# Kernel tuning notes

Hardware: AMD Instinct MI355X
Metric: run time of the kernel (lower is better)

## Reference

```python
import jax, jax.numpy as jnp
import numpy as np
import math

E = 2048; H = 16; NOPE = 128; ROPE = 64; VH = 128; C = 512; QR = 1536
DR = 2; BASE = 10000.0; LR = 4  # hypernet low_rank -> C//4 = 128
B = 2; S = 2048


def _ln(x, g, b):
    m = jnp.mean(x, axis=-1, keepdims=True)
    v = jnp.mean((x - m) ** 2, axis=-1, keepdims=True)
    return (x - m) / jnp.sqrt(v + 1e-5) * g + b


def _rope(x, sin, cos):
    # interleaved rotary: x[..., 0::2], x[..., 1::2]
    x1 = x[..., 0::2]
    x2 = x[..., 1::2]
    out = jnp.stack([x1 * cos - x2 * sin, x1 * sin + x2 * cos], axis=-1)
    return out.reshape(x.shape)


def _sincos(pos, dim):
    inv = BASE ** (-jnp.arange(0, dim, 2, dtype=jnp.float32) / dim)
    ang = pos[:, None] * inv  # [S, dim//2]
    return jnp.sin(ang), jnp.cos(ang)


def _pe(T, d):
    # sinusoidal positional encoding [T, d]
    pos = jnp.arange(T, dtype=jnp.float32)[:, None]
    div = jnp.exp(jnp.arange(0, d, 2, dtype=jnp.float32) * (-math.log(10000.0) / d))
    pe = jnp.zeros((T, d))
    pe = pe.at[:, 0::2].set(jnp.sin(pos * div))
    pe = pe.at[:, 1::2].set(jnp.cos(pos * div))
    return pe


def _forward(query, key, value, wq_a, q_ln_g, q_ln_b, wq_b, wkv_a, kv_ln_g,
             kv_ln_b, wkv_b, wo, fc_c_w, fc_c_b, fc_p_w, fc_p_b, pos_scale):
    B_, S_, _ = query.shape
    # LoRA query path
    ql = _ln(query @ wq_a.T, q_ln_g, q_ln_b)                 # [B,S,QR]
    q = (ql @ wq_b.T).reshape(B_, S_, H, NOPE + ROPE)
    q_nope, q_pe = q[..., :NOPE], q[..., NOPE:]
    # positions: start_pos = key_len - 1 (prefill entering incremental path)
    start = S_ - 1
    pos = jnp.arange(start, start + S_, dtype=jnp.float32)
    sin, cos = _sincos(pos, ROPE)                            # [S, ROPE//2]
    q_pe = _rope(q_pe, sin[None, :, None, :], cos[None, :, None, :])
    # KV latent path
    kvf = key @ wkv_a.T                                      # [B,S,C+ROPE]
    kv, k_pe = kvf[..., :C], kvf[..., C:]
    k_pe = _rope(k_pe, sin[None, :, :], cos[None, :, :])     # [B,S,ROPE]
    kvn = _ln(kv, kv_ln_g, kv_ln_b)                          # [B,S,C]
    # HyperNetwork temporal compression: W [B, t, T]
    T = S_
    t = math.ceil(T / DR)
    Cpe = _pe(t, C)                                          # [t, C]
    C2 = Cpe @ fc_c_w.T + fc_c_b                             # [t, C//LR]
    P2 = kvn @ fc_p_w.T + fc_p_b                             # [B,T,C//LR]
    W = jax.nn.sigmoid(jnp.einsum('tr,bTr->btT', C2, P2))    # [B,t,T]
    # chunk mask: compressed slot r gathers tokens in its down_rate chunk
    zm = (jnp.arange(T)[None, :] // DR == jnp.arange(t)[:, None]).astype(kvn.dtype)
    prev_kv = jnp.einsum('btT,bTc->btc', W * zm[None], kvn)  # [B,t,C]
    idx = list(range(DR - 1, T, DR))
    if T - 1 not in idx:
        idx.append(T - 1)
    prev_kpe = k_pe[:, np.array(idx)]                        # [B,t,ROPE]
    # LoRA-absorbed attention
    wkvb = wkv_b.reshape(H, NOPE + VH, C)
    qn = jnp.einsum('bshd,hdc->bshc', q_nope, wkvb[:, :NOPE])
    content = jnp.einsum('bshc,btc->bsht', qn, prev_kv)
    # decoupled (normalized) rope scores
    qpe_n = q_pe / jnp.maximum(jnp.linalg.norm(q_pe, axis=-1, keepdims=True), 1e-12)
    kpe_n = prev_kpe / jnp.maximum(jnp.linalg.norm(prev_kpe, axis=-1, keepdims=True), 1e-12)
    pscore = jnp.einsum('bshr,btr->bsht', qpe_n, kpe_n)
    scores = (content + pos_scale * pscore) * ((NOPE + ROPE) ** -0.5)
    attn = jax.nn.softmax(scores, axis=-1)                   # [B,S,H,t]
    x = jnp.einsum('bsht,btc->bshc', attn, prev_kv)
    x = jnp.einsum('bshc,hdc->bshd', x, wkvb[:, NOPE:])      # value up-proj
    return x.reshape(B_, S_, H * VH) @ wo.T


def setup_inputs() -> dict:
    key = jax.random.key(0)
    ks = jax.random.split(key, 16)
    s = 0.02
    return {
        'query': jax.random.normal(ks[0], (B, S, E), jnp.float32),
        'key': jax.random.normal(ks[1], (B, S, E), jnp.float32),
        'value': jax.random.normal(ks[2], (B, S, E), jnp.float32),
        'wq_a': jax.random.normal(ks[3], (QR, E), jnp.float32) * s,
        'q_ln_g': jnp.ones((QR,), jnp.float32),
        'q_ln_b': jnp.zeros((QR,), jnp.float32),
        'wq_b': jax.random.normal(ks[4], (H * (NOPE + ROPE), QR), jnp.float32) * s,
        'wkv_a': jax.random.normal(ks[5], (C + ROPE, E), jnp.float32) * s,
        'kv_ln_g': jnp.ones((C,), jnp.float32),
        'kv_ln_b': jnp.zeros((C,), jnp.float32),
        'wkv_b': jax.random.normal(ks[6], (H * (NOPE + VH), C), jnp.float32) * s,
        'wo': jax.random.normal(ks[7], (E, H * VH), jnp.float32) * s,
        'fc_c_w': jax.random.normal(ks[8], (C // LR, C), jnp.float32) * s,
        'fc_c_b': jnp.zeros((C // LR,), jnp.float32),
        'fc_p_w': jax.random.normal(ks[9], (C // LR, C), jnp.float32) * s,
        'fc_p_b': jnp.zeros((C // LR,), jnp.float32),
        'pos_scale': jnp.asarray(1.0, jnp.float32),
    }


def reference(query, key, value, wq_a, q_ln_g, q_ln_b, wq_b, wkv_a, kv_ln_g,
              kv_ln_b, wkv_b, wo, fc_c_w, fc_c_b, fc_p_w, fc_p_b, pos_scale):
    return _forward(query, key, value, wq_a, q_ln_g, q_ln_b, wq_b, wkv_a,
                    kv_ln_g, kv_ln_b, wkv_b, wo, fc_c_w, fc_c_b, fc_p_w,
                    fc_p_b, pos_scale)
```

## Files before the change

kernel.cpp:

```cpp
#include <hip/hip_runtime.h>
#include <math.h>

#define S_ 2048
#define B_ 2
#define H_ 16
#define E_ 2048
#define QR_ 1536
#define NOPE_ 128
#define ROPE_ 64
#define C_ 512
#define VH_ 128
#define T_ 1024
#define LN1E4 9.210340371976184f
#define SCALE_ 0.07216878364870323f

typedef _Float16 half8 __attribute__((ext_vector_type(8)));
typedef _Float16 half4 __attribute__((ext_vector_type(4)));
typedef __fp16 fp16x2 __attribute__((ext_vector_type(2)));
typedef float floatx4 __attribute__((ext_vector_type(4)));
#define MFMA16(a, b, c) __builtin_amdgcn_mfma_f32_16x16x32_f16(a, b, c, 0, 0, 0)

__device__ __forceinline__ void gload16(const _Float16* g, _Float16* l) {
  __builtin_amdgcn_global_load_lds(
      (__attribute__((address_space(1))) const void*)g,
      (__attribute__((address_space(3))) void*)l, 16, 0, 0);
}

__device__ __forceinline__ int xcd_swizzle(int orig, int nwg) {
  int q8 = nwg >> 3, r8 = nwg & 7, xcd = orig & 7, base = orig >> 3;
  return (xcd < r8 ? xcd * (q8 + 1) : r8 * (q8 + 1) + (xcd - r8) * q8) + base;
}

__global__ __launch_bounds__(256) void conv_all(
    const float* __restrict__ q, const float* __restrict__ k,
    const float* __restrict__ wqa, const float* __restrict__ wqb,
    const float* __restrict__ wkva, const float* __restrict__ wo,
    const float* __restrict__ fcc, const float* __restrict__ fcp,
    const float* __restrict__ wkvb,
    _Float16* q16, _Float16* k16, _Float16* wqa16, _Float16* wqb16,
    _Float16* wkva16, _Float16* wo16, _Float16* fcc16, _Float16* fcp16,
    _Float16* W1c, _Float16* W2c)
{
  size_t i = (size_t)blockIdx.x * 256 + threadIdx.x;
  if (i >= 3768320) {
    bool isW1 = i < 3899392;
    size_t j = i - (isW1 ? 3768320 : 3899392);
    int cch = j & 63, hd = (int)(j >> 6);
    int hh = hd >> 7, dd = hd & 127;
    const float* src = wkvb + ((size_t)(hh * 256 + (isW1 ? 0 : 128) + dd)) * 512 + cch * 8;
    float sc = isW1 ? SCALE_ : 1.f;
    float4 a = *(const float4*)src;
    float4 b = *(const float4*)(src + 4);
    half8 h = {(_Float16)(a.x * sc), (_Float16)(a.y * sc), (_Float16)(a.z * sc),
               (_Float16)(a.w * sc), (_Float16)(b.x * sc), (_Float16)(b.y * sc),
               (_Float16)(b.z * sc), (_Float16)(b.w * sc)};
    *(half8*)((isW1 ? W1c : W2c) + j * 8) = h;
    return;
  }
  const float* in; _Float16* out; size_t off;
  if      (i < 1048576) { in = q;    out = q16;    off = i; }
  else if (i < 2097152) { in = k;    out = k16;    off = i - 1048576; }
  else if (i < 2490368) { in = wqa;  out = wqa16;  off = i - 2097152; }
  else if (i < 3080192) { in = wqb;  out = wqb16;  off = i - 2490368; }
  else if (i < 3227648) { in = wkva; out = wkva16; off = i - 3080192; }
  else if (i < 3751936) { in = wo;   out = wo16;   off = i - 3227648; }
  else if (i < 3760128) { in = fcc;  out = fcc16;  off = i - 3751936; }
  else                  { in = fcp;  out = fcp16;  off = i - 3760128; }
  float4 a = ((const float4*)in)[2 * off];
  float4 b = ((const float4*)in)[2 * off + 1];
  half8 h = {(_Float16)a.x, (_Float16)a.y, (_Float16)a.z, (_Float16)a.w,
             (_Float16)b.x, (_Float16)b.y, (_Float16)b.z, (_Float16)b.w};
  *(half8*)(out + 8 * off) = h;
}

template<bool OUT16, bool NB, bool BIAS, bool TRANSC, bool DUAL = false>
__global__ __launch_bounds__(256) void gemm16(
    const _Float16* __restrict__ A, const _Float16* __restrict__ Bm,
    const float* __restrict__ bias, const float* __restrict__ bias2,
    float* __restrict__ Cf, _Float16* __restrict__ Ch,
    int N, int K, int lda, int ldb, int ldc,
    long sAb, long sAh, long sBb, long sBh, long sCb, long sCh)
{
  __shared__ __align__(16) _Float16 Asl[2][128 * 64];
  __shared__ __align__(16) _Float16 Bsl[2][128 * 64];
  int mode = 0;
  if (DUAL) {
    int zz = blockIdx.z;
    mode = zz >> 5;
    int z2 = zz & 31;
    int zb2 = z2 >> 4, zh2 = z2 & 15;
    A += (size_t)zb2 * sAb;
    const _Float16* Bsel = mode ? (const _Float16*)bias2 : Bm;
    Bm = Bsel + (size_t)zh2 * (128 * C_);
    if (mode) Ch = ((_Float16*)Cf) + ((size_t)(zb2 * H_ + zh2) * 128) * T_;
    else      Ch += ((size_t)(zb2 * H_ + zh2) * T_) * 192;
  } else {
    const int z = blockIdx.z, zb = z >> 4, zh = z & 15;
    A  += (size_t)zb * sAb + (size_t)zh * sAh;
    Bm += (size_t)zb * sBb + (size_t)zh * sBh;
    if (OUT16) Ch += (size_t)zb * sCb + (size_t)zh * sCh;
    else       Cf += (size_t)zb * sCb + (size_t)zh * sCh;
  }
  const int gx = gridDim.x;
  const int nwg = gx * gridDim.y;
  const int f = xcd_swizzle(blockIdx.y * gx + blockIdx.x, nwg);
  const int bm = (f / gx) * 128, bn = (f % gx) * 128;
  const int tid = threadIdx.x;
  const int w = tid >> 6, lane = tid & 63, l15 = lane & 15, g = lane >> 4;
  const int wm = (w >> 1) * 64, wn = (w & 1) * 64;
  const int srow = w * 32 + (lane >> 3);
  const int sch  = (lane & 7) ^ (lane >> 3);
  floatx4 acc[4][4];
  #pragma unroll
  for (int i = 0; i < 4; ++i)
    #pragma unroll
    for (int j = 0; j < 4; ++j) acc[i][j] = (floatx4){0.f, 0.f, 0.f, 0.f};

  auto STAGE = [&](int buf, int k0) {
    _Float16* al = &Asl[buf][w * 2048];
    _Float16* bl = &Bsl[buf][w * 2048];
    #pragma unroll
    for (int i = 0; i < 4; ++i)
      gload16(A + (size_t)(bm + srow + i * 8) * lda + k0 + sch * 8, al + i * 512);
    #pragma unroll
    for (int i = 0; i < 4; ++i)
      gload16(Bm + (size_t)(bn + srow + i * 8) * ldb + k0 + sch * 8, bl + i * 512);
  };

  STAGE(0, 0);
  int cur = 0;
  const int nIter = K >> 6;
  for (int it = 0; it < nIter; ++it) {
    const bool pf = (it + 1 < nIter);
    if (pf) STAGE(cur ^ 1, (it + 1) << 6);
    if (pf) asm volatile("s_waitcnt vmcnt(8)" ::: "memory");
    else    asm volatile("s_waitcnt vmcnt(0)" ::: "memory");
    __builtin_amdgcn_sched_barrier(0);
    __builtin_amdgcn_s_barrier();
    __builtin_amdgcn_sched_barrier(0);
    #pragma unroll
    for (int kk = 0; kk < 2; ++kk) {
      half8 af[4], bf[4];
      const int sw = ((kk * 4 + g) ^ (l15 & 7)) * 8;
      #pragma unroll
      for (int i = 0; i < 4; ++i) {
        af[i] = *(const half8*)&Asl[cur][(wm + i * 16 + l15) * 64 + sw];
        bf[i] = *(const half8*)&Bsl[cur][(wn + i * 16 + l15) * 64 + sw];
      }
      #pragma unroll
      for (int i = 0; i < 4; ++i)
        #pragma unroll
        for (int j = 0; j < 4; ++j)
          acc[i][j] = MFMA16(af[i], bf[j], acc[i][j]);
    }
    asm volatile("s_waitcnt lgkmcnt(0)" ::: "memory");
    __builtin_amdgcn_sched_barrier(0);
    __builtin_amdgcn_s_barrier();
    __builtin_amdgcn_sched_barrier(0);
    cur ^= 1;
  }

  if (DUAL) {
    if (mode) {
      #pragma unroll
      for (int i = 0; i < 4; ++i)
        #pragma unroll
        for (int j = 0; j < 4; ++j) {
          int row = bm + wm + i * 16 + g * 4;
          int col = wn + j * 16 + l15;
          half4 v = {(_Float16)acc[i][j][0], (_Float16)acc[i][j][1],
                     (_Float16)acc[i][j][2], (_Float16)acc[i][j][3]};
          *(half4*)(Ch + (size_t)col * T_ + row) = v;
        }
    } else {
      #pragma unroll
      for (int i = 0; i < 4; ++i)
        #pragma unroll
        for (int j = 0; j < 4; ++j)
          #pragma unroll
          for (int r = 0; r < 4; ++r) {
            int row = bm + wm + i * 16 + g * 4 + r;
            int col = wn + j * 16 + l15;
            Ch[(size_t)row * 192 + col] = (_Float16)acc[i][j][r];
          }
    }
  } else if (TRANSC) {
    #pragma unroll
    for (int i = 0; i < 4; ++i)
      #pragma unroll
      for (int j = 0; j < 4; ++j) {
        int row = bm + wm + i * 16 + g * 4;
        int col = bn + wn + j * 16 + l15;
        half4 v = {(_Float16)acc[i][j][0], (_Float16)acc[i][j][1],
                   (_Float16)acc[i][j][2], (_Float16)acc[i][j][3]};
        *(half4*)(Ch + (size_t)col * ldc + row) = v;
      }
  } else {
    #pragma unroll
    for (int i = 0; i < 4; ++i)
      #pragma unroll
      for (int j = 0; j < 4; ++j)
        #pragma unroll
        for (int r = 0; r < 4; ++r) {
          int row = bm + wm + i * 16 + g * 4 + r;
          int col = bn + wn + j * 16 + l15;
          if (!NB || col < N) {
            float v = acc[i][j][r];
            if (BIAS) v += (col < 128) ? bias[col] : bias2[col - 128];
            if (OUT16) Ch[(size_t)row * ldc + col] = (_Float16)v;
            else       Cf[(size_t)row * ldc + col] = v;
          }
        }
  }
}

template<typename TIN, bool OUT16>
__global__ __launch_bounds__(256) void ln_rows(
    const TIN* __restrict__ in, float* __restrict__ outf, _Float16* __restrict__ outh,
    const float* __restrict__ g, const float* __restrict__ bb,
    int L, int ldin, int ldout)
{
  const int row = blockIdx.x;
  const TIN* x = in + (size_t)row * ldin;
  float s = 0.f, s2 = 0.f;
  for (int i = threadIdx.x; i < L; i += 256) {
    float v = (float)x[i]; s += v; s2 += v * v;
  }
  #pragma unroll
  for (int off = 32; off; off >>= 1) {
    s  += __shfl_xor(s, off, 64);
    s2 += __shfl_xor(s2, off, 64);
  }
  __shared__ float rs[4], rs2[4];
  int lane = threadIdx.x & 63, w = threadIdx.x >> 6;
  if (lane == 0) { rs[w] = s; rs2[w] = s2; }
  __syncthreads();
  s  = rs[0] + rs[1] + rs[2] + rs[3];
  s2 = rs2[0] + rs2[1] + rs2[2] + rs2[3];
  float mean = s / L;
  float var = s2 / L - mean * mean;
  float inv = rsqrtf(var + 1e-5f);
  for (int i = threadIdx.x; i < L; i += 256) {
    float v = ((float)x[i] - mean) * inv * g[i] + bb[i];
    if (OUT16) outh[(size_t)row * ldout + i] = (_Float16)v;
    else       outf[(size_t)row * ldout + i] = v;
  }
}

__global__ __launch_bounds__(256) void rope_q16(_Float16* __restrict__ qb,
                                                const float* __restrict__ ps_ptr)
{
  const int row = blockIdx.x;
  const int s = row & (S_ - 1);
  const int lane = threadIdx.x & 63, w = threadIdx.x >> 6;
  float sn = 0.f, cs = 0.f;
  if (lane < 32) {
    float invf = expf(-(float)lane * (LN1E4 / 32.f));
    float ang = (float)(S_ - 1 + s) * invf;
    sincosf(ang, &sn, &cs);
  }
  const float psc = ps_ptr[0] * SCALE_;
  #pragma unroll
  for (int hh = 0; hh < 4; ++hh) {
    const int h = w + hh * 4;
    _Float16* p = qb + (size_t)row * 3072 + h * 192 + NOPE_;
    float o1 = 0.f, o2 = 0.f;
    if (lane < 32) {
      float x1 = (float)p[2 * lane], x2 = (float)p[2 * lane + 1];
      o1 = x1 * cs - x2 * sn;
      o2 = x1 * sn + x2 * cs;
    }
    float ss = o1 * o1 + o2 * o2;
    #pragma unroll
    for (int off = 32; off; off >>= 1) ss += __shfl_xor(ss, off, 64);
    float inv = psc / fmaxf(sqrtf(ss), 1e-12f);
    if (lane < 32) {
      p[2 * lane]     = (_Float16)(o1 * inv);
      p[2 * lane + 1] = (_Float16)(o2 * inv);
    }
  }
}

__global__ __launch_bounds__(64) void rope_k16(
    const _Float16* __restrict__ kvf16, _Float16* __restrict__ keff)
{
  const int t = blockIdx.x, b = blockIdx.y;
  const int srow = 2 * t + 1;
  const _Float16* p = kvf16 + ((size_t)(b * S_ + srow)) * 576 + C_;
  const int j = threadIdx.x;
  float o1 = 0.f, o2 = 0.f;
  if (j < 32) {
    float invf = expf(-(float)j * (LN1E4 / 32.f));
    float ang = (float)(S_ - 1 + srow) * invf;
    float sn, cs; sincosf(ang, &sn, &cs);
    float x1 = (float)p[2 * j], x2 = (float)p[2 * j + 1];
    o1 = x1 * cs - x2 * sn;
    o2 = x1 * sn + x2 * cs;
  }
  float ss = o1 * o1 + o2 * o2;
  #pragma unroll
  for (int off = 32; off; off >>= 1) ss += __shfl_xor(ss, off, 64);
  float nrm = fmaxf(sqrtf(ss), 1e-12f);
  if (j < 32) {
    _Float16 h1 = (_Float16)(o1 / nrm), h2 = (_Float16)(o2 / nrm);
    #pragma unroll
    for (int h = 0; h < H_; ++h) {
      _Float16* o = keff + ((size_t)((b * H_ + h) * T_) + t) * 192 + NOPE_;
      o[2 * j] = h1; o[2 * j + 1] = h2;
    }
  }
}

__global__ __launch_bounds__(256) void pe16(_Float16* __restrict__ Cpe16)
{
  const int t = blockIdx.x;
  const int i = threadIdx.x;
  float dv = expf(-(float)(2 * i) * (LN1E4 / 512.f));
  float ang = (float)t * dv;
  float sn, cs; sincosf(ang, &sn, &cs);
  Cpe16[(size_t)t * C_ + 2 * i]     = (_Float16)sn;
  Cpe16[(size_t)t * C_ + 2 * i + 1] = (_Float16)cs;
}

__global__ __launch_bounds__(64) void gate_kernel(
    const _Float16* __restrict__ Ccat, const _Float16* __restrict__ kvn16,
    _Float16* __restrict__ pkv16)
{
  const int t = blockIdx.x, b = blockIdx.y;
  const int j = threadIdx.x;
  const _Float16* c2 = Ccat + (size_t)t * 256;
  const _Float16* p0 = Ccat + (size_t)(1024 + b * S_ + 2 * t) * 256 + 128;
  const _Float16* p1 = p0 + 256;
  float d0 = (float)c2[j] * (float)p0[j] + (float)c2[j + 64] * (float)p0[j + 64];
  float d1 = (float)c2[j] * (float)p1[j] + (float)c2[j + 64] * (float)p1[j + 64];
  #pragma unroll
  for (int off = 32; off; off >>= 1) {
    d0 += __shfl_xor(d0, off, 64);
    d1 += __shfl_xor(d1, off, 64);
  }
  float w0 = 1.f / (1.f + expf(-d0));
  float w1 = 1.f / (1.f + expf(-d1));
  const _Float16* k0 = kvn16 + ((size_t)(b * S_ + 2 * t)) * C_;
  const _Float16* k1 = k0 + C_;
  _Float16* o = pkv16 + ((size_t)(b * T_ + t)) * C_;
  #pragma unroll
  for (int it = 0; it < 2; ++it) {
    int c = j * 4 + it * 256;
    half4 a = *(const half4*)(k0 + c);
    half4 bb = *(const half4*)(k1 + c);
    half4 r;
    #pragma unroll
    for (int u = 0; u < 4; ++u)
      r[u] = (_Float16)(w0 * (float)a[u] + w1 * (float)bb[u]);
    *(half4*)(o + c) = r;
  }
}

__global__ __launch_bounds__(256, 3) void attn_flash(
    const _Float16* __restrict__ qb16, const _Float16* __restrict__ keff,
    const _Float16* __restrict__ vT, _Float16* __restrict__ x216)
{
  __shared__ __align__(16) _Float16 K_lds[64 * 192];
  __shared__ __align__(16) _Float16 V_lds[128 * 64];
  const int f = xcd_swizzle(blockIdx.x, 1024);
  const int st = f & 31, h = (f >> 5) & 15, b = f >> 9;
  const int tid = threadIdx.x, w = tid >> 6, lane = tid & 63;
  const int l15 = lane & 15, g = lane >> 4, l7 = lane & 7;
  const int rq = b * S_ + st * 64 + w * 16;
  const _Float16* qrow = qb16 + (size_t)(rq + l15) * 3072 + h * 192;
  half8 qB[6];
  #pragma unroll
  for (int kk = 0; kk < 6; ++kk) qB[kk] = *(const half8*)(qrow + kk * 32 + g * 8);
  floatx4 O[8];
  #pragma unroll
  for (int i = 0; i < 8; ++i) O[i] = (floatx4){0.f, 0.f, 0.f, 0.f};
  float m = -3e38f, l = 0.f;
  const _Float16* kb = keff + (size_t)(b * H_ + h) * T_ * 192;
  const _Float16* vb = vT   + (size_t)(b * H_ + h) * 128 * T_;

  int ksrc[6], ksw[6], vsrc[4], vsw[4];
  #pragma unroll
  for (int p = 0; p < 6; ++p) {
    int c = tid + p * 256;
    int r = c / 24, dc = c % 24;
    ksrc[p] = r * 192 + dc * 8;
    ksw[p]  = r * 192 + ((dc ^ (r & 7)) * 8);
  }
  #pragma unroll
  for (int p = 0; p < 4; ++p) {
    int c = tid + p * 256;
    int r = c >> 3, dc = c & 7;
    vsrc[p] = r * T_ + dc * 8;
    vsw[p]  = r * 64 + ((dc ^ (r & 7)) * 8);
  }
  int kswr[6], vswr[2];
  #pragma unroll
  for (int kk = 0; kk < 6; ++kk) kswr[kk] = ((kk * 4 + g) ^ l7) * 8;
  #pragma unroll
  for (int kc = 0; kc < 2; ++kc) vswr[kc] = ((kc * 4 + g) ^ l7) * 8;

  half8 kreg[6], vreg[4];
  #pragma unroll
  for (int p = 0; p < 6; ++p) kreg[p] = *(const half8*)(kb + ksrc[p]);
  #pragma unroll
  for (int p = 0; p < 4; ++p) vreg[p] = *(const half8*)(vb + vsrc[p]);
  #pragma unroll
  for (int p = 0; p < 6; ++p) *(half8*)&K_lds[ksw[p]] = kreg[p];
  #pragma unroll
  for (int p = 0; p < 4; ++p) *(half8*)&V_lds[vsw[p]] = vreg[p];
  __syncthreads();

  const int srcA = l15 + ((g & 1) << 5);
  const int srcB = srcA + 16;
  const bool hi = (g >> 1) != 0;

  for (int kt = 0; kt < 16; ++kt) {
    if (kt < 15) {
      const int t1 = (kt + 1) * 64;
      #pragma unroll
      for (int p = 0; p < 6; ++p)
        kreg[p] = *(const half8*)(kb + (size_t)t1 * 192 + ksrc[p]);
      #pragma unroll
      for (int p = 0; p < 4; ++p)
        vreg[p] = *(const half8*)(vb + t1 + vsrc[p]);
    }
    floatx4 sc[4];
    #pragma unroll
    for (int i = 0; i < 4; ++i) sc[i] = (floatx4){0.f, 0.f, 0.f, 0.f};
    __builtin_amdgcn_s_setprio(1);
    #pragma unroll
    for (int kk = 0; kk < 6; ++kk)
      #pragma unroll
      for (int ct = 0; ct < 4; ++ct)
        sc[ct] = MFMA16(
            *(const half8*)&K_lds[(ct * 16 + l15) * 192 + kswr[kk]],
            qB[kk], sc[ct]);
    __builtin_amdgcn_s_setprio(0);
    float pm = sc[0][0];
    #pragma unroll
    for (int ct = 0; ct < 4; ++ct)
      #pragma unroll
      for (int r = 0; r < 4; ++r) pm = fmaxf(pm, sc[ct][r]);
    pm = fmaxf(pm, __shfl_xor(pm, 16, 64));
    pm = fmaxf(pm, __shfl_xor(pm, 32, 64));
    int ok = pm <= m + 8.f;
    if (!__all(ok)) {
      float mn = fmaxf(m, pm);
      float sf = __expf(m - mn);
      m = mn; l *= sf;
      float sfO[4];
      #pragma unroll
      for (int r = 0; r < 4; ++r) sfO[r] = __shfl(sf, g * 4 + r, 64);
      #pragma unroll
      for (int cc = 0; cc < 8; ++cc) {
        O[cc][0] *= sfO[0]; O[cc][1] *= sfO[1];
        O[cc][2] *= sfO[2]; O[cc][3] *= sfO[3];
      }
    }
    float rs = 0.f;
    #pragma unroll
    for (int ct = 0; ct < 4; ++ct)
      #pragma unroll
      for (int r = 0; r < 4; ++r) {
        float e = __expf(sc[ct][r] - m);
        sc[ct][r] = e; rs += e;
      }
    rs += __shfl_xor(rs, 16, 64);
    rs += __shfl_xor(rs, 32, 64);
    l += rs;
    unsigned pk[4][2];
    #pragma unroll
    for (int ct = 0; ct < 4; ++ct) {
      union { fp16x2 h; unsigned u; } c0, c1;
      c0.h = __builtin_amdgcn_cvt_pkrtz(sc[ct][0], sc[ct][1]);
      c1.h = __builtin_amdgcn_cvt_pkrtz(sc[ct][2], sc[ct][3]);
      pk[ct][0] = c0.u; pk[ct][1] = c1.u;
    }
    __builtin_amdgcn_s_setprio(1);
    #pragma unroll
    for (int kc = 0; kc < 2; ++kc) {
      unsigned a0 = __shfl((int)pk[2 * kc][0], srcA, 64);
      unsigned b0 = __shfl((int)pk[2 * kc + 1][0], srcA, 64);
      unsigned a1 = __shfl((int)pk[2 * kc][1], srcA, 64);
      unsigned b1 = __shfl((int)pk[2 * kc + 1][1], srcA, 64);
      unsigned a2 = __shfl((int)pk[2 * kc][0], srcB, 64);
      unsigned b2 = __shfl((int)pk[2 * kc + 1][0], srcB, 64);
      unsigned a3 = __shfl((int)pk[2 * kc][1], srcB, 64);
      unsigned b3 = __shfl((int)pk[2 * kc + 1][1], srcB, 64);
      union { unsigned u[4]; half8 h; } pa;
      pa.u[0] = hi ? b0 : a0;
      pa.u[1] = hi ? b1 : a1;
      pa.u[2] = hi ? b2 : a2;
      pa.u[3] = hi ? b3 : a3;
      #pragma unroll
      for (int cc = 0; cc < 8; ++cc)
        O[cc] = MFMA16(pa.h,
            *(const half8*)&V_lds[(cc * 16 + l15) * 64 + vswr[kc]], O[cc]);
    }
    __builtin_amdgcn_s_setprio(0);
    if (kt < 15) {
      __syncthreads();
      #pragma unroll
      for (int p = 0; p < 6; ++p) *(half8*)&K_lds[ksw[p]] = kreg[p];
      #pragma unroll
      for (int p = 0; p < 4; ++p) *(half8*)&V_lds[vsw[p]] = vreg[p];
      __syncthreads();
    }
  }
  float il = 1.f / l;
  float ilO[4];
  #pragma unroll
  for (int r = 0; r < 4; ++r) ilO[r] = __shfl(il, g * 4 + r, 64);
  #pragma unroll
  for (int cc = 0; cc < 8; ++cc)
    #pragma unroll
    for (int r = 0; r < 4; ++r)
      x216[(size_t)(rq + g * 4 + r) * 2048 + h * 128 + cc * 16 + l15] =
          (_Float16)(O[cc][r] * ilO[r]);
}

extern "C" void kernel_launch(void* const* d_in, const int* in_sizes, int n_in,
                              void* d_out, int out_size, void* d_ws, size_t ws_size,
                              hipStream_t stream)
{
  (void)in_sizes; (void)n_in; (void)out_size; (void)ws_size;
  const float* query  = (const float*)d_in[0];
  const float* key    = (const float*)d_in[1];
  const float* wq_a   = (const float*)d_in[3];
  const float* q_ln_g = (const float*)d_in[4];
  const float* q_ln_b = (const float*)d_in[5];
  const float* wq_b   = (const float*)d_in[6];
  const float* wkv_a  = (const float*)d_in[7];
  const float* kv_ln_g= (const float*)d_in[8];
  const float* kv_ln_b= (const float*)d_in[9];
  const float* wkvb   = (const float*)d_in[10];
  const float* wo     = (const float*)d_in[11];
  const float* fc_c_w = (const float*)d_in[12];
  const float* fc_c_b = (const float*)d_in[13];
  const float* fc_p_w = (const float*)d_in[14];
  const float* fc_p_b = (const float*)d_in[15];
  const float* ps     = (const float*)d_in[16];
  float* out = (float*)d_out;

  const int M = B_ * S_;
  _Float16* hws   = (_Float16*)d_ws;
  _Float16* q16   = hws;
  _Float16* key16 = q16   + (size_t)8388608;
  _Float16* wqa16 = key16 + (size_t)8388608;
  _Float16* wqb16 = wqa16 + (size_t)3145728;
  _Float16* wkva16= wqb16 + (size_t)4718592;
  _Float16* wo16  = wkva16+ (size_t)1179648;
  _Float16* ql16  = wo16  + (size_t)4194304;
  _Float16* qb16  = ql16  + (size_t)6291456;
  _Float16* kvf16 = qb16  + (size_t)12582912;
  _Float16* kvn16 = kvf16 + (size_t)2359296;
  _Float16* fcc16 = kvn16 + (size_t)2097152;
  _Float16* fcp16 = fcc16 + (size_t)65536;
  _Float16* W1c   = fcp16 + (size_t)65536;
  _Float16* W2c   = W1c   + (size_t)1048576;
  _Float16* x216  = q16;
  _Float16* keff  = key16;
  _Float16* Cpe16 = kvn16 - (size_t)524288;
  _Float16* Ccat  = wqb16;
  _Float16* pkv16 = wkva16;
  _Float16* vT    = ql16;

  conv_all<<<15744, 256, 0, stream>>>(query, key, wq_a, wq_b, wkv_a, wo, fc_c_w, fc_p_w,
                                      wkvb, q16, key16, wqa16, wqb16, wkva16, wo16,
                                      fcc16, fcp16, W1c, W2c);
  gemm16<true,false,false,false><<<dim3(QR_/128, M/128), 256, 0, stream>>>(
      q16, wqa16, nullptr, nullptr, nullptr, ql16, QR_, E_, E_, E_, QR_, 0,0,0,0,0,0);
  ln_rows<_Float16,true><<<M, 256, 0, stream>>>(ql16, nullptr, ql16, q_ln_g, q_ln_b,
                                                QR_, QR_, QR_);
  gemm16<true,false,false,false><<<dim3(3072/128, M/128), 256, 0, stream>>>(
      ql16, wqb16, nullptr, nullptr, nullptr, qb16, 3072, QR_, QR_, QR_, 3072, 0,0,0,0,0,0);
  rope_q16<<<M, 256, 0, stream>>>(qb16, ps);
  gemm16<true,true,false,false><<<dim3(5, M/128), 256, 0, stream>>>(
      key16, wkva16, nullptr, nullptr, nullptr, kvf16, 576, E_, E_, E_, 576, 0,0,0,0,0,0);
  ln_rows<_Float16,true><<<M, 256, 0, stream>>>(kvf16, nullptr, kvn16, kv_ln_g, kv_ln_b,
                                                C_, 576, C_);
  rope_k16<<<dim3(T_, B_), 64, 0, stream>>>(kvf16, keff);
  pe16<<<T_, 256, 0, stream>>>(Cpe16);
  gemm16<true,false,true,false><<<dim3(2, 5120/128), 256, 0, stream>>>(
      Cpe16, fcc16, fc_c_b, fc_p_b, nullptr, Ccat, 256, C_, C_, C_, 256, 0,0,0,0,0,0);
  gate_kernel<<<dim3(T_, B_), 64, 0, stream>>>(Ccat, kvn16, pkv16);
  gemm16<true,false,false,false,true><<<dim3(1, T_/128, 64), 256, 0, stream>>>(
      pkv16, W1c, nullptr, (const float*)W2c, (float*)vT, keff,
      128, C_, C_, C_, 192, (long)T_*C_, 0L, 0L, 0L, 0L, 0L);
  attn_flash<<<dim3(1024), 256, 0, stream>>>(qb16, keff, vT, x216);
  gemm16<false,false,false,false><<<dim3(E_/128, M/128), 256, 0, stream>>>(
      x216, wo16, nullptr, nullptr, out, nullptr, E_, E_, E_, E_, E_, 0,0,0,0,0,0);
}
```

Baseline: 345.2 us.

## Batch independent GEMMs and elementwise kernels into fewer multi-task launches

Independent GEMMs (q-down with kv-down, and q-up with hypernet C-projection) are merged into one launch each through a task-dispatching gemm_pair kernel. The two layernorms, k-rope and PE generation are merged into one kernel, and q-rope is merged with the gating kernel. Workspace buffers are reassigned so the merged stages do not alias. The aim is to cut launch count and fill the GPU better with small GEMMs running next to large ones. The cost is more branching and a generic GEMM without the templated specialisations.

```diff
diff --git a/kernel.cpp b/kernel.cpp
--- a/kernel.cpp
+++ b/kernel.cpp
@@ -214,58 +214,142 @@
   }
 }
 
-template<typename TIN, bool OUT16>
-__global__ __launch_bounds__(256) void ln_rows(
-    const TIN* __restrict__ in, float* __restrict__ outf, _Float16* __restrict__ outh,
-    const float* __restrict__ g, const float* __restrict__ bb,
-    int L, int ldin, int ldout)
+struct GTask {
+  const _Float16* A; const _Float16* B; _Float16* C;
+  const float* b1; const float* b2;
+  int gx, N, K, lda, ldb, ldc;
+};
+
+__global__ __launch_bounds__(256) void gemm_pair(GTask ta, GTask tb, int n0, int n1)
 {
-  const int row = blockIdx.x;
-  const TIN* x = in + (size_t)row * ldin;
-  float s = 0.f, s2 = 0.f;
-  for (int i = threadIdx.x; i < L; i += 256) {
-    float v = (float)x[i]; s += v; s2 += v * v;
-  }
-  #pragma unroll
-  for (int off = 32; off; off >>= 1) {
-    s  += __shfl_xor(s, off, 64);
-    s2 += __shfl_xor(s2, off, 64);
-  }
+  __shared__ __align__(16) _Float16 Asl[2][128 * 64];
+  __shared__ __align__(16) _Float16 Bsl[2][128 * 64];
+  const bool second = blockIdx.x >= (unsigned)n0;
+  GTask t = second ? tb : ta;
+  const int fid = second ? blockIdx.x - n0 : blockIdx.x;
+  const int nwg = second ? n1 : n0;
+  const int f = xcd_swizzle(fid, nwg);
+  const int bm = (f / t.gx) * 128, bn = (f % t.gx) * 128;
+  const int tid = threadIdx.x;
+  const int w = tid >> 6, lane = tid & 63, l15 = lane & 15, g = lane >> 4;
+  const int wm = (w >> 1) * 64, wn = (w & 1) * 64;
+  const int srow = w * 32 + (lane >> 3);
+  const int sch  = (lane & 7) ^ (lane >> 3);
+  floatx4 acc[4][4];
+  #pragma unroll
+  for (int i = 0; i < 4; ++i)
+    #pragma unroll
+    for (int j = 0; j < 4; ++j) acc[i][j] = (floatx4){0.f, 0.f, 0.f, 0.f};
+
+  auto STAGE = [&](int buf, int k0) {
+    _Float16* al = &Asl[buf][w * 2048];
+    _Float16* bl = &Bsl[buf][w * 2048];
+    #pragma unroll
+    for (int i = 0; i < 4; ++i)
+      gload16(t.A + (size_t)(bm + srow + i * 8) * t.lda + k0 + sch * 8, al + i * 512);
+    #pragma unroll
+    for (int i = 0; i < 4; ++i)
+      gload16(t.B + (size_t)(bn + srow + i * 8) * t.ldb + k0 + sch * 8, bl + i * 512);
+  };
+
+  STAGE(0, 0);
+  int cur = 0;
+  const int nIter = t.K >> 6;
+  for (int it = 0; it < nIter; ++it) {
+    const bool pf = (it + 1 < nIter);
+    if (pf) STAGE(cur ^ 1, (it + 1) << 6);
+    if (pf) asm volatile("s_waitcnt vmcnt(8)" ::: "memory");
+    else    asm volatile("s_waitcnt vmcnt(0)" ::: "memory");
+    __builtin_amdgcn_sched_barrier(0);
+    __builtin_amdgcn_s_barrier();
+    __builtin_amdgcn_sched_barrier(0);
+    #pragma unroll
+    for (int kk = 0; kk < 2; ++kk) {
+      half8 af[4], bf[4];
+      const int sw = ((kk * 4 + g) ^ (l15 & 7)) * 8;
+      #pragma unroll
+      for (int i = 0; i < 4; ++i) {
+        af[i] = *(const half8*)&Asl[cur][(wm + i * 16 + l15) * 64 + sw];
+        bf[i] = *(const half8*)&Bsl[cur][(wn + i * 16 + l15) * 64 + sw];
+      }
+      #pragma unroll
+      for (int i = 0; i < 4; ++i)
+        #pragma unroll
+        for (int j = 0; j < 4; ++j)
+          acc[i][j] = MFMA16(af[i], bf[j], acc[i][j]);
+    }
+    asm volatile("s_waitcnt lgkmcnt(0)" ::: "memory");
+    __builtin_amdgcn_sched_barrier(0);
+    __builtin_amdgcn_s_barrier();
+    __builtin_amdgcn_sched_barrier(0);
+    cur ^= 1;
+  }
+  #pragma unroll
+  for (int i = 0; i < 4; ++i)
+    #pragma unroll
+    for (int j = 0; j < 4; ++j)
+      #pragma unroll
+      for (int r = 0; r < 4; ++r) {
+        int row = bm + wm + i * 16 + g * 4 + r;
+        int col = bn + wn + j * 16 + l15;
+        if (col < t.N) {
+          float v = acc[i][j][r];
+          if (t.b1) v += (col < 128) ? t.b1[col] : t.b2[col - 128];
+          t.C[(size_t)row * t.ldc + col] = (_Float16)v;
+        }
+      }
+}
+
+__global__ __launch_bounds__(256) void fused_ln(
+    _Float16* __restrict__ ql16, const _Float16* __restrict__ kvf16,
+    _Float16* __restrict__ kvnA,
+    const float* __restrict__ qg, const float* __restrict__ qb,
+    const float* __restrict__ kg, const float* __restrict__ kb,
+    _Float16* __restrict__ keff, _Float16* __restrict__ Cpe16)
+{
   __shared__ float rs[4], rs2[4];
-  int lane = threadIdx.x & 63, w = threadIdx.x >> 6;
-  if (lane == 0) { rs[w] = s; rs2[w] = s2; }
-  __syncthreads();
-  s  = rs[0] + rs[1] + rs[2] + rs[3];
-  s2 = rs2[0] + rs2[1] + rs2[2] + rs2[3];
-  float mean = s / L;
-  float var = s2 / L - mean * mean;
-  float inv = rsqrtf(var + 1e-5f);
-  for (int i = threadIdx.x; i < L; i += 256) {
-    float v = ((float)x[i] - mean) * inv * g[i] + bb[i];
-    if (OUT16) outh[(size_t)row * ldout + i] = (_Float16)v;
-    else       outf[(size_t)row * ldout + i] = v;
-  }
-}
-
-__global__ __launch_bounds__(256) void rope_q16(_Float16* __restrict__ qb,
-                                                const float* __restrict__ ps_ptr)
-{
-  const int row = blockIdx.x;
-  const int s = row & (S_ - 1);
-  const int lane = threadIdx.x & 63, w = threadIdx.x >> 6;
-  float sn = 0.f, cs = 0.f;
-  if (lane < 32) {
-    float invf = expf(-(float)lane * (LN1E4 / 32.f));
-    float ang = (float)(S_ - 1 + s) * invf;
-    sincosf(ang, &sn, &cs);
-  }
-  const float psc = ps_ptr[0] * SCALE_;
-  #pragma unroll
-  for (int hh = 0; hh < 4; ++hh) {
-    const int h = w + hh * 4;
-    _Float16* p = qb + (size_t)row * 3072 + h * 192 + NOPE_;
+  int bid = blockIdx.x;
+  const int tid = threadIdx.x;
+  const int lane = tid & 63, w = tid >> 6;
+  if (bid < 8192) {
+    const bool isQ = bid < 4096;
+    const int row = isQ ? bid : bid - 4096;
+    const _Float16* x = isQ ? ql16 + (size_t)row * 1536 : kvf16 + (size_t)row * 576;
+    _Float16* o = isQ ? ql16 + (size_t)row * 1536 : kvnA + (size_t)row * 512;
+    const float* g_ = isQ ? qg : kg;
+    const float* b_ = isQ ? qb : kb;
+    const int L = isQ ? 1536 : 512;
+    float s = 0.f, s2 = 0.f;
+    for (int i = tid; i < L; i += 256) {
+      float v = (float)x[i]; s += v; s2 += v * v;
+    }
+    #pragma unroll
+    for (int off = 32; off; off >>= 1) {
+      s  += __shfl_xor(s, off, 64);
+      s2 += __shfl_xor(s2, off, 64);
+    }
+    if (lane == 0) { rs[w] = s; rs2[w] = s2; }
+    __syncthreads();
+    s  = rs[0] + rs[1] + rs[2] + rs[3];
+    s2 = rs2[0] + rs2[1] + rs2[2] + rs2[3];
+    float mean = s / L;
+    float var = s2 / L - mean * mean;
+    float inv = rsqrtf(var + 1e-5f);
+    for (int i = tid; i < L; i += 256)
+      o[i] = (_Float16)(((float)x[i] - mean) * inv * g_[i] + b_[i]);
+    return;
+  }
+  bid -= 8192;
+  if (bid < 512) {
+    int u = bid * 4 + w;
+    int t = u & (T_ - 1), b = u >> 10;
+    const int srow = 2 * t + 1;
+    const _Float16* p = kvf16 + ((size_t)(b * S_ + srow)) * 576 + C_;
     float o1 = 0.f, o2 = 0.f;
     if (lane < 32) {
+      float invf = expf(-(float)lane * (LN1E4 / 32.f));
+      float ang = (float)(S_ - 1 + srow) * invf;
+      float sn, cs; sincosf(ang, &sn, &cs);
       float x1 = (float)p[2 * lane], x2 = (float)p[2 * lane + 1];
       o1 = x1 * cs - x2 * sn;
       o2 = x1 * sn + x2 * cs;
@@ -273,86 +357,98 @@
     float ss = o1 * o1 + o2 * o2;
     #pragma unroll
     for (int off = 32; off; off >>= 1) ss += __shfl_xor(ss, off, 64);
-    float inv = psc / fmaxf(sqrtf(ss), 1e-12f);
+    float nrm = fmaxf(sqrtf(ss), 1e-12f);
     if (lane < 32) {
-      p[2 * lane]     = (_Float16)(o1 * inv);
-      p[2 * lane + 1] = (_Float16)(o2 * inv);
-    }
-  }
-}
-
-__global__ __launch_bounds__(64) void rope_k16(
-    const _Float16* __restrict__ kvf16, _Float16* __restrict__ keff)
-{
-  const int t = blockIdx.x, b = blockIdx.y;
-  const int srow = 2 * t + 1;
-  const _Float16* p = kvf16 + ((size_t)(b * S_ + srow)) * 576 + C_;
-  const int j = threadIdx.x;
-  float o1 = 0.f, o2 = 0.f;
-  if (j < 32) {
-    float invf = expf(-(float)j * (LN1E4 / 32.f));
-    float ang = (float)(S_ - 1 + srow) * invf;
+      _Float16 h1 = (_Float16)(o1 / nrm), h2 = (_Float16)(o2 / nrm);
+      #pragma unroll
+      for (int h = 0; h < H_; ++h) {
+        _Float16* o = keff + ((size_t)((b * H_ + h) * T_) + t) * 192 + NOPE_;
+        o[2 * lane] = h1; o[2 * lane + 1] = h2;
+      }
+    }
+    return;
+  }
+  bid -= 512;
+  {
+    const int t = bid;
+    float dv = expf(-(float)(2 * tid) * (LN1E4 / 512.f));
+    float ang = (float)t * dv;
     float sn, cs; sincosf(ang, &sn, &cs);
-    float x1 = (float)p[2 * j], x2 = (float)p[2 * j + 1];
-    o1 = x1 * cs - x2 * sn;
-    o2 = x1 * sn + x2 * cs;
-  }
-  float ss = o1 * o1 + o2 * o2;
-  #pragma unroll
-  for (int off = 32; off; off >>= 1) ss += __shfl_xor(ss, off, 64);
-  float nrm = fmaxf(sqrtf(ss), 1e-12f);
-  if (j < 32) {
-    _Float16 h1 = (_Float16)(o1 / nrm), h2 = (_Float16)(o2 / nrm);
-    #pragma unroll
-    for (int h = 0; h < H_; ++h) {
-      _Float16* o = keff + ((size_t)((b * H_ + h) * T_) + t) * 192 + NOPE_;
-      o[2 * j] = h1; o[2 * j + 1] = h2;
-    }
-  }
-}
-
-__global__ __launch_bounds__(256) void pe16(_Float16* __restrict__ Cpe16)
-{
-  const int t = blockIdx.x;
-  const int i = threadIdx.x;
-  float dv = expf(-(float)(2 * i) * (LN1E4 / 512.f));
-  float ang = (float)t * dv;
-  float sn, cs; sincosf(ang, &sn, &cs);
-  Cpe16[(size_t)t * C_ + 2 * i]     = (_Float16)sn;
-  Cpe16[(size_t)t * C_ + 2 * i + 1] = (_Float16)cs;
-}
-
-__global__ __launch_bounds__(64) void gate_kernel(
-    const _Float16* __restrict__ Ccat, const _Float16* __restrict__ kvn16,
+    Cpe16[(size_t)t * C_ + 2 * tid]     = (_Float16)sn;
+    Cpe16[(size_t)t * C_ + 2 * tid + 1] = (_Float16)cs;
+  }
+}
+
+__global__ __launch_bounds__(256) void fused_rq_gate(
+    _Float16* __restrict__ qb16, const float* __restrict__ ps_ptr,
+    const _Float16* __restrict__ Ccat, const _Float16* __restrict__ kvnA,
     _Float16* __restrict__ pkv16)
 {
-  const int t = blockIdx.x, b = blockIdx.y;
-  const int j = threadIdx.x;
-  const _Float16* c2 = Ccat + (size_t)t * 256;
-  const _Float16* p0 = Ccat + (size_t)(1024 + b * S_ + 2 * t) * 256 + 128;
-  const _Float16* p1 = p0 + 256;
-  float d0 = (float)c2[j] * (float)p0[j] + (float)c2[j + 64] * (float)p0[j + 64];
-  float d1 = (float)c2[j] * (float)p1[j] + (float)c2[j + 64] * (float)p1[j + 64];
-  #pragma unroll
-  for (int off = 32; off; off >>= 1) {
-    d0 += __shfl_xor(d0, off, 64);
-    d1 += __shfl_xor(d1, off, 64);
-  }
-  float w0 = 1.f / (1.f + expf(-d0));
-  float w1 = 1.f / (1.f + expf(-d1));
-  const _Float16* k0 = kvn16 + ((size_t)(b * S_ + 2 * t)) * C_;
-  const _Float16* k1 = k0 + C_;
-  _Float16* o = pkv16 + ((size_t)(b * T_ + t)) * C_;
-  #pragma unroll
-  for (int it = 0; it < 2; ++it) {
-    int c = j * 4 + it * 256;
-    half4 a = *(const half4*)(k0 + c);
-    half4 bb = *(const half4*)(k1 + c);
-    half4 r;
-    #pragma unroll
-    for (int u = 0; u < 4; ++u)
-      r[u] = (_Float16)(w0 * (float)a[u] + w1 * (float)bb[u]);
-    *(half4*)(o + c) = r;
+  int bid = blockIdx.x;
+  const int tid = threadIdx.x;
+  const int lane = tid & 63, w = tid >> 6;
+  if (bid < 4096) {
+    const int row = bid;
+    const int s = row & (S_ - 1);
+    float sn = 0.f, cs = 0.f;
+    if (lane < 32) {
+      float invf = expf(-(float)lane * (LN1E4 / 32.f));
+      float ang = (float)(S_ - 1 + s) * invf;
+      sincosf(ang, &sn, &cs);
+    }
+    const float psc = ps_ptr[0] * SCALE_;
+    #pragma unroll
+    for (int hh = 0; hh < 4; ++hh) {
+      const int h = w + hh * 4;
+      _Float16* p = qb16 + (size_t)row * 3072 + h * 192 + NOPE_;
+      float o1 = 0.f, o2 = 0.f;
+      if (lane < 32) {
+        float x1 = (float)p[2 * lane], x2 = (float)p[2 * lane + 1];
+        o1 = x1 * cs - x2 * sn;
+        o2 = x1 * sn + x2 * cs;
+      }
+      float ss = o1 * o1 + o2 * o2;
+      #pragma unroll
+      for (int off = 32; off; off >>= 1) ss += __shfl_xor(ss, off, 64);
+      float inv = psc / fmaxf(sqrtf(ss), 1e-12f);
+      if (lane < 32) {
+        p[2 * lane]     = (_Float16)(o1 * inv);
+        p[2 * lane + 1] = (_Float16)(o2 * inv);
+      }
+    }
+    return;
+  }
+  bid -= 4096;
+  {
+    int u = bid * 4 + w;
+    int t = u & (T_ - 1), b = u >> 10;
+    const int j = lane;
+    const _Float16* c2 = Ccat + (size_t)t * 256;
+    const _Float16* p0 = Ccat + (size_t)(1024 + b * S_ + 2 * t) * 256 + 128;
+    const _Float16* p1 = p0 + 256;
+    float d0 = (float)c2[j] * (float)p0[j] + (float)c2[j + 64] * (float)p0[j + 64];
+    float d1 = (float)c2[j] * (float)p1[j] + (float)c2[j + 64] * (float)p1[j + 64];
+    #pragma unroll
+    for (int off = 32; off; off >>= 1) {
+      d0 += __shfl_xor(d0, off, 64);
+      d1 += __shfl_xor(d1, off, 64);
+    }
+    float w0 = 1.f / (1.f + expf(-d0));
+    float w1 = 1.f / (1.f + expf(-d1));
+    const _Float16* k0 = kvnA + ((size_t)(b * S_ + 2 * t)) * C_;
+    const _Float16* k1 = k0 + C_;
+    _Float16* o = pkv16 + ((size_t)(b * T_ + t)) * C_;
+    #pragma unroll
+    for (int it = 0; it < 2; ++it) {
+      int c = j * 4 + it * 256;
+      half4 a = *(const half4*)(k0 + c);
+      half4 bb = *(const half4*)(k1 + c);
+      half4 r;
+      #pragma unroll
+      for (int uu = 0; uu < 4; ++uu)
+        r[uu] = (_Float16)(w0 * (float)a[uu] + w1 * (float)bb[uu]);
+      *(half4*)(o + c) = r;
+    }
   }
 }
 
@@ -560,30 +656,28 @@
   _Float16* W2c   = W1c   + (size_t)1048576;
   _Float16* x216  = q16;
   _Float16* keff  = key16;
-  _Float16* Cpe16 = kvn16 - (size_t)524288;
-  _Float16* Ccat  = wqb16;
+  _Float16* Cpe16 = q16;
+  _Float16* kvnA  = q16 + (size_t)524288;
+  _Float16* Ccat  = wqa16;
   _Float16* pkv16 = wkva16;
   _Float16* vT    = ql16;
 
   conv_all<<<15744, 256, 0, stream>>>(query, key, wq_a, wq_b, wkv_a, wo, fc_c_w, fc_p_w,
                                       wkvb, q16, key16, wqa16, wqb16, wkva16, wo16,
                                       fcc16, fcp16, W1c, W2c);
-  gemm16<true,false,false,false><<<dim3(QR_/128, M/128), 256, 0, stream>>>(
-      q16, wqa16, nullptr, nullptr, nullptr, ql16, QR_, E_, E_, E_, QR_, 0,0,0,0,0,0);
-  ln_rows<_Float16,true><<<M, 256, 0, stream>>>(ql16, nullptr, ql16, q_ln_g, q_ln_b,
-                                                QR_, QR_, QR_);
-  gemm16<true,false,false,false><<<dim3(3072/128, M/128), 256, 0, stream>>>(
-      ql16, wqb16, nullptr, nullptr, nullptr, qb16, 3072, QR_, QR_, QR_, 3072, 0,0,0,0,0,0);
-  rope_q16<<<M, 256, 0, stream>>>(qb16, ps);
-  gemm16<true,true,false,false><<<dim3(5, M/128), 256, 0, stream>>>(
-      key16, wkva16, nullptr, nullptr, nullptr, kvf16, 576, E_, E_, E_, 576, 0,0,0,0,0,0);
-  ln_rows<_Float16,true><<<M, 256, 0, stream>>>(kvf16, nullptr, kvn16, kv_ln_g, kv_ln_b,
-                                                C_, 576, C_);
-  rope_k16<<<dim3(T_, B_), 64, 0, stream>>>(kvf16, keff);
-  pe16<<<T_, 256, 0, stream>>>(Cpe16);
-  gemm16<true,false,true,false><<<dim3(2, 5120/128), 256, 0, stream>>>(
-      Cpe16, fcc16, fc_c_b, fc_p_b, nullptr, Ccat, 256, C_, C_, C_, 256, 0,0,0,0,0,0);
-  gate_kernel<<<dim3(T_, B_), 64, 0, stream>>>(Ccat, kvn16, pkv16);
+  {
+    GTask ta = {q16,   wqa16,  ql16,  nullptr, nullptr, 12, QR_, E_, E_, E_, QR_};
+    GTask tb = {key16, wkva16, kvf16, nullptr, nullptr, 5,  576, E_, E_, E_, 576};
+    gemm_pair<<<544, 256, 0, stream>>>(ta, tb, 384, 160);
+  }
+  fused_ln<<<9728, 256, 0, stream>>>(ql16, kvf16, kvnA, q_ln_g, q_ln_b,
+                                     kv_ln_g, kv_ln_b, keff, Cpe16);
+  {
+    GTask ta = {ql16,  wqb16, qb16, nullptr, nullptr, 24, 3072, QR_, QR_, QR_, 3072};
+    GTask tb = {Cpe16, fcc16, Ccat, fc_c_b,  fc_p_b,  2,  256,  C_,  C_,  C_,  256};
+    gemm_pair<<<848, 256, 0, stream>>>(ta, tb, 768, 80);
+  }
+  fused_rq_gate<<<4608, 256, 0, stream>>>(qb16, ps, Ccat, kvnA, pkv16);
   gemm16<true,false,false,false,true><<<dim3(1, T_/128, 64), 256, 0, stream>>>(
       pkv16, W1c, nullptr, (const float*)W2c, (float*)vT, keff,
       128, C_, C_, C_, 192, (long)T_*C_, 0L, 0L, 0L, 0L, 0L);
```

New measurement: 326.9 us. 5.3% less time.
